# Kernel optimization log

Hardware: AMD Instinct MI355X
Metric: run time of the kernel (lower is better)

The kernel has to match this reference:

```python
import jax, jax.numpy as jnp
import numpy as np

B, F, D = 16384, 32, 64
EPS = 1e-5


def layer_norm(x, g, b):
    m = x.mean(-1, keepdims=True)
    v = ((x - m) ** 2).mean(-1, keepdims=True)
    return (x - m) / jnp.sqrt(v + EPS) * g + b


def setup_inputs() -> dict:
    key = jax.random.key(0)
    ks = jax.random.split(key, 24)
    IN = F * D

    def w(k, shape, fan_in):
        return jax.random.normal(k, shape, dtype=jnp.float32) / np.sqrt(fan_in)

    return {
        "x": jax.random.normal(ks[0], (B, F, D), dtype=jnp.float32),
        # StaticGRN (mask branch): Linear(IN,D) -> ELU -> Linear(D,F); skip Linear(IN,F); GateAndNorm(F)
        "mw1": w(ks[1], (IN, D), IN), "mb1": jnp.zeros((D,), jnp.float32),
        "mw2": w(ks[2], (D, F), D), "mb2": jnp.zeros((F,), jnp.float32),
        "mlw": w(ks[3], (IN, F), IN), "mlb": jnp.zeros((F,), jnp.float32),
        "mgw": w(ks[4], (F, F), F), "mgb": jnp.zeros((F,), jnp.float32),
        "mlw2": w(ks[5], (F, F), F), "mlb2": jnp.zeros((F,), jnp.float32),
        "mgamma": jnp.ones((F,), jnp.float32), "mbeta": jnp.zeros((F,), jnp.float32),
        # Per-feature GRNNoContext params, stacked over F (batched small GEMMs)
        "w1": w(ks[6], (F, D, D), D), "b1": jnp.zeros((F, D), jnp.float32),
        "w2": w(ks[7], (F, D, D), D), "b2": jnp.zeros((F, D), jnp.float32),
        "gw": w(ks[8], (F, D, D), D), "gb": jnp.zeros((F, D), jnp.float32),
        "lw": w(ks[9], (F, D, D), D), "lb": jnp.zeros((F, D), jnp.float32),
        "gamma": jnp.ones((F, D), jnp.float32), "beta": jnp.zeros((F, D), jnp.float32),
    }


def reference(x, mw1, mb1, mw2, mb2, mlw, mlb, mgw, mgb, mlw2, mlb2, mgamma, mbeta,
              w1, b1, w2, b2, gw, gb, lw, lb, gamma, beta):
    b, f, d = x.shape
    flat = x.reshape(b, f * d)
    # StaticGRN mask branch (dropout is 0.0 -> identity)
    h = jax.nn.elu(flat @ mw1 + mb1) @ mw2 + mb2          # [B,F]
    res = flat @ mlw + mlb                                 # [B,F] skip path
    pre = jax.nn.sigmoid(h @ mgw + mgb) * (h @ mlw2 + mlb2) + res
    mask = jax.nn.softmax(layer_norm(pre, mgamma, mbeta), axis=-1)[:, None, :]  # [B,1,F]
    # Per-feature GRNs, batched over the feature axis
    hh = jax.nn.elu(jnp.einsum('bfd,fde->bfe', x, w1) + b1)
    hh = jnp.einsum('bfd,fde->bfe', hh, w2) + b2
    gate = jax.nn.sigmoid(jnp.einsum('bfd,fde->bfe', hh, gw) + gb)
    lin = jnp.einsum('bfd,fde->bfe', hh, lw) + lb
    vecs = layer_norm(gate * lin + x, gamma, beta)         # [B,F,D]
    out = jnp.einsum('bof,bfd->bod', mask, vecs)[:, 0, :]  # [B,D]
    return out, mask
```

## Files before the change

kernel.cpp:

```cpp
#include <hip/hip_runtime.h>
#include <hip/hip_bf16.h>
#include <math.h>

#define NB 16384
#define NF 32
#define ND 64
#define NIN 2048

typedef __attribute__((ext_vector_type(8))) short fragA;
typedef __attribute__((ext_vector_type(4))) float fragC;

#define MFMA(a, b, c) __builtin_amdgcn_mfma_f32_16x16x32_bf16((a), (b), (c), 0, 0, 0)

__device__ __forceinline__ short f2bf(float f) {
    union { float f; unsigned u; } v; v.f = f;
    return (short)((v.u + 0x7fffu + ((v.u >> 16) & 1u)) >> 16);
}
__device__ __forceinline__ fragA cvt8(const float* p) {
    const float4 a = *(const float4*)p;
    const float4 b = *(const float4*)(p + 4);
    union { __hip_bfloat162 h[4]; fragA f; } u;
    u.h[0] = __float22bfloat162_rn(make_float2(a.x, a.y));
    u.h[1] = __float22bfloat162_rn(make_float2(a.z, a.w));
    u.h[2] = __float22bfloat162_rn(make_float2(b.x, b.y));
    u.h[3] = __float22bfloat162_rn(make_float2(b.z, b.w));
    return u.f;
}

__device__ __forceinline__ float frcp(float x) { return __builtin_amdgcn_rcpf(x); }
__device__ __forceinline__ float felu(float v) { return v > 0.f ? v : __expf(v) - 1.f; }
__device__ __forceinline__ float fsig(float g) { return __builtin_amdgcn_rcpf(1.f + __expf(-g)); }

__global__ __launch_bounds__(256) void prep_kernel(
    const float* __restrict__ w1, const float* __restrict__ w2,
    const float* __restrict__ gw, const float* __restrict__ lw,
    const float* __restrict__ mw1, const float* __restrict__ mlw,
    const float* __restrict__ mw2, const float* __restrict__ mgw,
    const float* __restrict__ mlw2,
    short* __restrict__ wsout)
{
    int F = blockIdx.x * 256 + threadIdx.x;
    fragA o;
    if (F < 65536) {
        int mat = F >> 14;
        int f   = (F >> 9) & 31;
        int nt  = (F >> 7) & 3;
        int s   = (F >> 6) & 1;
        int l   = F & 63;
        const float* src = (mat == 0 ? w1 : mat == 1 ? w2 : mat == 2 ? gw : lw)
                           + (size_t)f * 4096;
        int n  = nt * 16 + (l & 15);
        int k0 = s * 32 + ((l >> 4) << 3);
#pragma unroll
        for (int j = 0; j < 8; ++j) o[j] = f2bf(src[(k0 + j) * 64 + n]);
    } else if (F < 90112) {
        int G  = F - 65536;
        int f  = G / 768;
        int r  = G - f * 768;
        int nt = r >> 7;
        int s  = (r >> 6) & 1;
        int l  = r & 63;
        int n  = nt * 16 + (l & 15);
        int k0 = f * 64 + s * 32 + ((l >> 4) << 3);
        if (n < 64) {
#pragma unroll
            for (int j = 0; j < 8; ++j) o[j] = f2bf(mw1[(size_t)(k0 + j) * 64 + n]);
        } else {
#pragma unroll
            for (int j = 0; j < 8; ++j) o[j] = f2bf(mlw[(size_t)(k0 + j) * 32 + (n - 64)]);
        }
    } else {
        int G2 = F - 90112;
        if (G2 < 256) {
            int nt = G2 >> 7, s = (G2 >> 6) & 1, l = G2 & 63;
            int n = nt * 16 + (l & 15);
            int k0 = s * 32 + ((l >> 4) << 3);
#pragma unroll
            for (int j = 0; j < 8; ++j) o[j] = f2bf(mw2[(k0 + j) * 32 + n]);
        } else {
            int G3 = G2 - 256;
            const float* src = (G3 < 128) ? mgw : mlw2;
            G3 &= 127;
            int nt = G3 >> 6, l = G3 & 63;
            int n = nt * 16 + (l & 15);
            int k0 = (l >> 4) << 3;
#pragma unroll
            for (int j = 0; j < 8; ++j) o[j] = f2bf(src[(k0 + j) * 32 + n]);
        }
    }
    ((fragA*)wsout)[F] = o;
}

__global__ __launch_bounds__(256, 4) void fused_kernel(
    const float* __restrict__ x,
    const short* __restrict__ wfrag, const short* __restrict__ mwfrag,
    const short* __restrict__ swfrag,
    const float* __restrict__ mb1, const float* __restrict__ mb2,
    const float* __restrict__ mlb, const float* __restrict__ mgb,
    const float* __restrict__ mlb2,
    const float* __restrict__ mgamma, const float* __restrict__ mbeta,
    const float* __restrict__ b1, const float* __restrict__ b2,
    const float* __restrict__ gb, const float* __restrict__ lb,
    const float* __restrict__ gamma, const float* __restrict__ beta,
    float* __restrict__ mask_out, float* __restrict__ out)
{
    __shared__ float smem[8960];
    float* redS  = smem;
    float* gS    = smem;
    float* lS    = smem + 768;
    float* hS1   = smem + 6208;
    float* resS  = smem + 7296;
    float* h2S   = smem + 7872;
    float* outS  = smem + 4352;
    float* maskS = smem + 8448;

    const int tid = threadIdx.x;
    const int w = tid >> 6, l = tid & 63;
    const int row0 = blockIdx.x * 16;
    const int m = l & 15, q = l >> 4;

    const fragA* wf  = (const fragA*)wfrag;
    const fragA* mwf = (const fragA*)mwfrag;
    const fragA* swf = (const fragA*)swfrag;

    fragC acc[6];
#pragma unroll
    for (int nt = 0; nt < 6; ++nt) acc[nt] = (fragC){0.f, 0.f, 0.f, 0.f};

    const float* xpm = x + (size_t)(row0 + m) * NIN + q * 8;
    for (int fi = 0; fi < 8; ++fi) {
        int f = w * 8 + fi;
        const float* xp = xpm + f * ND;
        fragA a0 = cvt8(xp), a1 = cvt8(xp + 32);
        const size_t fb = (size_t)f * 768 + l;
#pragma unroll
        for (int nt = 0; nt < 6; ++nt) {
            acc[nt] = MFMA(a0, mwf[fb + nt * 128], acc[nt]);
            acc[nt] = MFMA(a1, mwf[fb + nt * 128 + 64], acc[nt]);
        }
    }
    {
        float* myred = redS + w * 1552;
#pragma unroll
        for (int nt = 0; nt < 6; ++nt)
#pragma unroll
            for (int rg = 0; rg < 4; ++rg)
                myred[(q * 4 + rg) * 97 + nt * 16 + m] = acc[nt][rg];
    }
    __syncthreads();

    {
        int r = tid & 15, cb = tid >> 4;
#pragma unroll
        for (int i = 0; i < 6; ++i) {
            int c = cb + i * 16;
            float s = redS[r * 97 + c]        + redS[1552 + r * 97 + c]
                    + redS[3104 + r * 97 + c] + redS[4656 + r * 97 + c];
            if (c < 64) {
                hS1[r * 68 + c] = felu(s + mb1[c]);
            } else {
                resS[r * 36 + (c - 64)] = s + mlb[c - 64];
            }
        }
    }
    __syncthreads();

    if (w < 2) {
        const float* ap = hS1 + m * 68 + q * 8;
        fragA a0 = cvt8(ap), a1 = cvt8(ap + 32);
        fragC c = {0.f, 0.f, 0.f, 0.f};
        c = MFMA(a0, swf[w * 128 + l], c);
        c = MFMA(a1, swf[w * 128 + 64 + l], c);
        float bv = mb2[w * 16 + m];
#pragma unroll
        for (int rg = 0; rg < 4; ++rg)
            h2S[(q * 4 + rg) * 36 + w * 16 + m] = c[rg] + bv;
    }
    __syncthreads();

    {
        int ntc = w & 1;
        int isl = w >> 1;
        fragA a = cvt8(h2S + m * 36 + q * 8);
        fragC c = {0.f, 0.f, 0.f, 0.f};
        c = MFMA(a, swf[256 + isl * 128 + ntc * 64 + l], c);
        float* dst = isl ? lS : gS;
#pragma unroll
        for (int rg = 0; rg < 4; ++rg)
            dst[(q * 4 + rg) * 36 + ntc * 16 + m] = c[rg];
    }
    __syncthreads();

    if (w == 0) {
        int r2 = l >> 2, c0 = (l & 3) * 8;
        float pre[8];
#pragma unroll
        for (int i = 0; i < 8; ++i) {
            int c = c0 + i;
            float gg = gS[r2 * 36 + c] + mgb[c];
            float ll = lS[r2 * 36 + c] + mlb2[c];
            pre[i] = ll * fsig(gg) + resS[r2 * 36 + c];
        }
        float s1 = 0.f, s2 = 0.f;
#pragma unroll
        for (int i = 0; i < 8; ++i) { s1 += pre[i]; s2 += pre[i] * pre[i]; }
        s1 += __shfl_xor(s1, 1); s2 += __shfl_xor(s2, 1);
        s1 += __shfl_xor(s1, 2); s2 += __shfl_xor(s2, 2);
        float mean = s1 * (1.f / 32.f);
        float var  = s2 * (1.f / 32.f) - mean * mean;
        float inv  = rsqrtf(fmaxf(var, 0.f) + 1e-5f);
        float ln[8]; float mx = -3.4e38f;
#pragma unroll
        for (int i = 0; i < 8; ++i) {
            ln[i] = (pre[i] - mean) * inv * mgamma[c0 + i] + mbeta[c0 + i];
            mx = fmaxf(mx, ln[i]);
        }
        mx = fmaxf(mx, __shfl_xor(mx, 1));
        mx = fmaxf(mx, __shfl_xor(mx, 2));
        float ssum = 0.f;
#pragma unroll
        for (int i = 0; i < 8; ++i) { ln[i] = __expf(ln[i] - mx); ssum += ln[i]; }
        ssum += __shfl_xor(ssum, 1); ssum += __shfl_xor(ssum, 2);
        float rs = frcp(ssum);
        float* mo = mask_out + (size_t)(row0 + r2) * 32 + c0;
        *(float4*)mo       = (float4){ln[0] * rs, ln[1] * rs, ln[2] * rs, ln[3] * rs};
        *(float4*)(mo + 4) = (float4){ln[4] * rs, ln[5] * rs, ln[6] * rs, ln[7] * rs};
#pragma unroll
        for (int i = 0; i < 8; ++i) maskS[r2 * 32 + c0 + i] = ln[i] * rs;
    }
    __syncthreads();

    float* hW = smem + w * 1088;

    fragC oac[4];
#pragma unroll
    for (int nt = 0; nt < 4; ++nt) oac[nt] = (fragC){0.f, 0.f, 0.f, 0.f};

    for (int fi = 0; fi < 8; ++fi) {
        const int f = w * 8 + fi;
        const size_t base1 = (size_t)f * 512 + l;
        const size_t base2 = (size_t)(NF + f) * 512 + l;
        const size_t baseg = (size_t)(2 * NF + f) * 512 + l;
        const size_t basel = (size_t)(3 * NF + f) * 512 + l;

        const float* xp = xpm + f * ND;
        fragA a0 = cvt8(xp), a1 = cvt8(xp + 32);
        fragC c1[4];
#pragma unroll
        for (int nt = 0; nt < 4; ++nt) {
            fragC c = {0.f, 0.f, 0.f, 0.f};
            c = MFMA(a0, wf[base1 + nt * 128], c);
            c = MFMA(a1, wf[base1 + nt * 128 + 64], c);
            c1[nt] = c;
        }
        fragA w2f[8];
#pragma unroll
        for (int j = 0; j < 4; ++j) {
            w2f[j]     = wf[base2 + j * 128];
            w2f[j + 4] = wf[base2 + j * 128 + 64];
        }
#pragma unroll
        for (int nt = 0; nt < 4; ++nt) {
            float bv = b1[f * 64 + nt * 16 + m];
            int col = nt * 16 + m;
#pragma unroll
            for (int rg = 0; rg < 4; ++rg)
                hW[(q * 4 + rg) * 68 + col] = felu(c1[nt][rg] + bv);
        }
        const float* ap = hW + m * 68 + q * 8;
        fragA h0 = cvt8(ap), h1 = cvt8(ap + 32);
        fragC c2[4];
#pragma unroll
        for (int nt = 0; nt < 4; ++nt) {
            fragC c = {0.f, 0.f, 0.f, 0.f};
            c = MFMA(h0, w2f[nt], c);
            c = MFMA(h1, w2f[nt + 4], c);
            c2[nt] = c;
        }
        float xres[4][4];
#pragma unroll
        for (int rg = 0; rg < 4; ++rg)
#pragma unroll
            for (int nt = 0; nt < 4; ++nt)
                xres[rg][nt] = x[(size_t)(row0 + q * 4 + rg) * NIN + f * ND + nt * 16 + m];
        float mk[4];
#pragma unroll
        for (int rg = 0; rg < 4; ++rg) mk[rg] = maskS[(q * 4 + rg) * 32 + f];
#pragma unroll
        for (int nt = 0; nt < 4; ++nt) {
            float bv = b2[f * 64 + nt * 16 + m];
            int col = nt * 16 + m;
#pragma unroll
            for (int rg = 0; rg < 4; ++rg)
                hW[(q * 4 + rg) * 68 + col] = c2[nt][rg] + bv;
        }
        const float* ap2 = hW + m * 68 + q * 8;
        fragA g0 = cvt8(ap2), g1 = cvt8(ap2 + 32);
        fragC ga[4], la[4];
#pragma unroll
        for (int nt = 0; nt < 4; ++nt) {
            fragC g = {0.f, 0.f, 0.f, 0.f}, li = {0.f, 0.f, 0.f, 0.f};
            g  = MFMA(g0, wf[baseg + nt * 128], g);
            g  = MFMA(g1, wf[baseg + nt * 128 + 64], g);
            li = MFMA(g0, wf[basel + nt * 128], li);
            li = MFMA(g1, wf[basel + nt * 128 + 64], li);
            ga[nt] = g; la[nt] = li;
        }
        float gbv[4], lbv[4], gmv[4], btv[4];
#pragma unroll
        for (int nt = 0; nt < 4; ++nt) {
            int cidx = f * 64 + nt * 16 + m;
            gbv[nt] = gb[cidx]; lbv[nt] = lb[cidx];
            gmv[nt] = gamma[cidx]; btv[nt] = beta[cidx];
        }
#pragma unroll
        for (int rg = 0; rg < 4; ++rg) {
            float val[4];
#pragma unroll
            for (int nt = 0; nt < 4; ++nt) {
                float gg = ga[nt][rg] + gbv[nt];
                float ll = la[nt][rg] + lbv[nt];
                val[nt] = ll * fsig(gg) + xres[rg][nt];
            }
            float s1 = 0.f, s2 = 0.f;
#pragma unroll
            for (int nt = 0; nt < 4; ++nt) { s1 += val[nt]; s2 += val[nt] * val[nt]; }
            s1 += __shfl_xor(s1, 1); s2 += __shfl_xor(s2, 1);
            s1 += __shfl_xor(s1, 2); s2 += __shfl_xor(s2, 2);
            s1 += __shfl_xor(s1, 4); s2 += __shfl_xor(s2, 4);
            s1 += __shfl_xor(s1, 8); s2 += __shfl_xor(s2, 8);
            float mean = s1 * (1.f / 64.f);
            float var  = s2 * (1.f / 64.f) - mean * mean;
            float inv  = rsqrtf(fmaxf(var, 0.f) + 1e-5f);
#pragma unroll
            for (int nt = 0; nt < 4; ++nt) {
                float vec = (val[nt] - mean) * inv * gmv[nt] + btv[nt];
                oac[nt][rg] += mk[rg] * vec;
            }
        }
    }

#pragma unroll
    for (int nt = 0; nt < 4; ++nt)
#pragma unroll
        for (int rg = 0; rg < 4; ++rg)
            outS[w * 1024 + (q * 4 + rg) * 64 + nt * 16 + m] = oac[nt][rg];
    __syncthreads();
    {
        int t4 = tid * 4;
        int r = t4 >> 6, c = t4 & 63;
        float v[4];
#pragma unroll
        for (int j = 0; j < 4; ++j) {
            v[j] = outS[r * 64 + c + j] + outS[1024 + r * 64 + c + j]
                 + outS[2048 + r * 64 + c + j] + outS[3072 + r * 64 + c + j];
        }
        *(float4*)(out + (size_t)(row0 + r) * 64 + c) = (float4){v[0], v[1], v[2], v[3]};
    }
}

extern "C" void kernel_launch(void* const* d_in, const int* in_sizes, int n_in,
                              void* d_out, int out_size, void* d_ws, size_t ws_size,
                              hipStream_t stream) {
    const float* x      = (const float*)d_in[0];
    const float* mw1    = (const float*)d_in[1];
    const float* mb1    = (const float*)d_in[2];
    const float* mw2    = (const float*)d_in[3];
    const float* mb2    = (const float*)d_in[4];
    const float* mlw    = (const float*)d_in[5];
    const float* mlb    = (const float*)d_in[6];
    const float* mgw    = (const float*)d_in[7];
    const float* mgb    = (const float*)d_in[8];
    const float* mlw2   = (const float*)d_in[9];
    const float* mlb2   = (const float*)d_in[10];
    const float* mgamma = (const float*)d_in[11];
    const float* mbeta  = (const float*)d_in[12];
    const float* w1     = (const float*)d_in[13];
    const float* b1     = (const float*)d_in[14];
    const float* w2     = (const float*)d_in[15];
    const float* b2     = (const float*)d_in[16];
    const float* gw     = (const float*)d_in[17];
    const float* gb     = (const float*)d_in[18];
    const float* lw     = (const float*)d_in[19];
    const float* lb     = (const float*)d_in[20];
    const float* gamma  = (const float*)d_in[21];
    const float* beta   = (const float*)d_in[22];

    float* out  = (float*)d_out;
    float* mask = out + (size_t)NB * 64;

    short* wfrag  = (short*)d_ws;
    short* mwfrag = wfrag + (size_t)65536 * 8;
    short* swfrag = wfrag + (size_t)90112 * 8;

    hipLaunchKernelGGL(prep_kernel, dim3(354), dim3(256), 0, stream,
                       w1, w2, gw, lw, mw1, mlw, mw2, mgw, mlw2, wfrag);
    hipLaunchKernelGGL(fused_kernel, dim3(NB / 16), dim3(256), 0, stream,
                       x, wfrag, mwfrag, swfrag,
                       mb1, mb2, mlb, mgb, mlb2, mgamma, mbeta,
                       b1, b2, gb, lb, gamma, beta,
                       mask, out);
}
```

Before: 310.5 us.

## Double block to eight waves and split mask GEMM and feature loop across them

Launches the fused kernel with 512 threads (8 waves) instead of 256. The mask-branch GEMM is split so each group of four waves computes half of the output tiles. The per-feature GRN loop now gives each wave 4 features instead of 8, and the final output reduction sums 8 partial results. Shared-memory offsets are rearranged, and an extra barrier protects the reused output buffer. The goal is more in-flight waves per block to hide latency. The risks are heavier register limits from the tighter launch bounds, and x fragments being loaded twice in the mask GEMM.

```diff
diff --git a/kernel.cpp b/kernel.cpp
--- a/kernel.cpp
+++ b/kernel.cpp
@@ -91,7 +91,7 @@
     ((fragA*)wsout)[F] = o;
 }
 
-__global__ __launch_bounds__(256, 4) void fused_kernel(
+__global__ __launch_bounds__(512, 8) void fused_kernel(
     const float* __restrict__ x,
     const short* __restrict__ wfrag, const short* __restrict__ mwfrag,
     const short* __restrict__ swfrag,
@@ -104,15 +104,15 @@
     const float* __restrict__ gamma, const float* __restrict__ beta,
     float* __restrict__ mask_out, float* __restrict__ out)
 {
-    __shared__ float smem[8960];
+    __shared__ float smem[9216];
     float* redS  = smem;
     float* gS    = smem;
     float* lS    = smem + 768;
-    float* hS1   = smem + 6208;
-    float* resS  = smem + 7296;
-    float* h2S   = smem + 7872;
-    float* outS  = smem + 4352;
-    float* maskS = smem + 8448;
+    float* hS1   = smem + 6272;
+    float* resS  = smem + 7360;
+    float* h2S   = smem + 7936;
+    float* outS  = smem;
+    float* maskS = smem + 8704;
 
     const int tid = threadIdx.x;
     const int w = tid >> 6, l = tid & 63;
@@ -123,39 +123,44 @@
     const fragA* mwf = (const fragA*)mwfrag;
     const fragA* swf = (const fragA*)swfrag;
 
-    fragC acc[6];
-#pragma unroll
-    for (int nt = 0; nt < 6; ++nt) acc[nt] = (fragC){0.f, 0.f, 0.f, 0.f};
+    const int fs = (w & 3) * 8;
+    const int nh = w >> 2;
+    fragC acc[3];
+#pragma unroll
+    for (int j = 0; j < 3; ++j) acc[j] = (fragC){0.f, 0.f, 0.f, 0.f};
 
     const float* xpm = x + (size_t)(row0 + m) * NIN + q * 8;
     for (int fi = 0; fi < 8; ++fi) {
-        int f = w * 8 + fi;
+        int f = fs + fi;
         const float* xp = xpm + f * ND;
         fragA a0 = cvt8(xp), a1 = cvt8(xp + 32);
         const size_t fb = (size_t)f * 768 + l;
 #pragma unroll
-        for (int nt = 0; nt < 6; ++nt) {
-            acc[nt] = MFMA(a0, mwf[fb + nt * 128], acc[nt]);
-            acc[nt] = MFMA(a1, mwf[fb + nt * 128 + 64], acc[nt]);
+        for (int j = 0; j < 3; ++j) {
+            int nt = nh * 3 + j;
+            acc[j] = MFMA(a0, mwf[fb + nt * 128], acc[j]);
+            acc[j] = MFMA(a1, mwf[fb + nt * 128 + 64], acc[j]);
         }
     }
     {
-        float* myred = redS + w * 1552;
-#pragma unroll
-        for (int nt = 0; nt < 6; ++nt)
+        float* myred = redS + w * 784;
+#pragma unroll
+        for (int j = 0; j < 3; ++j)
 #pragma unroll
             for (int rg = 0; rg < 4; ++rg)
-                myred[(q * 4 + rg) * 97 + nt * 16 + m] = acc[nt][rg];
+                myred[(q * 4 + rg) * 49 + j * 16 + m] = acc[j][rg];
     }
     __syncthreads();
 
     {
         int r = tid & 15, cb = tid >> 4;
 #pragma unroll
-        for (int i = 0; i < 6; ++i) {
-            int c = cb + i * 16;
-            float s = redS[r * 97 + c]        + redS[1552 + r * 97 + c]
-                    + redS[3104 + r * 97 + c] + redS[4656 + r * 97 + c];
+        for (int i = 0; i < 3; ++i) {
+            int c = cb + i * 32;
+            int nh2 = (c >= 48) ? 1 : 0;
+            int base = nh2 * 3136 + r * 49 + (c - nh2 * 48);
+            float s = redS[base] + redS[base + 784]
+                    + redS[base + 1568] + redS[base + 2352];
             if (c < 64) {
                 hS1[r * 68 + c] = felu(s + mb1[c]);
             } else {
@@ -178,7 +183,7 @@
     }
     __syncthreads();
 
-    {
+    if (w < 4) {
         int ntc = w & 1;
         int isl = w >> 1;
         fragA a = cvt8(h2S + m * 36 + q * 8);
@@ -236,8 +241,8 @@
 #pragma unroll
     for (int nt = 0; nt < 4; ++nt) oac[nt] = (fragC){0.f, 0.f, 0.f, 0.f};
 
-    for (int fi = 0; fi < 8; ++fi) {
-        const int f = w * 8 + fi;
+    for (int fi = 0; fi < 4; ++fi) {
+        const int f = w * 4 + fi;
         const size_t base1 = (size_t)f * 512 + l;
         const size_t base2 = (size_t)(NF + f) * 512 + l;
         const size_t baseg = (size_t)(2 * NF + f) * 512 + l;
@@ -340,6 +345,7 @@
         }
     }
 
+    __syncthreads();
 #pragma unroll
     for (int nt = 0; nt < 4; ++nt)
 #pragma unroll
@@ -347,15 +353,15 @@
             outS[w * 1024 + (q * 4 + rg) * 64 + nt * 16 + m] = oac[nt][rg];
     __syncthreads();
     {
-        int t4 = tid * 4;
-        int r = t4 >> 6, c = t4 & 63;
-        float v[4];
-#pragma unroll
-        for (int j = 0; j < 4; ++j) {
-            v[j] = outS[r * 64 + c + j] + outS[1024 + r * 64 + c + j]
-                 + outS[2048 + r * 64 + c + j] + outS[3072 + r * 64 + c + j];
-        }
-        *(float4*)(out + (size_t)(row0 + r) * 64 + c) = (float4){v[0], v[1], v[2], v[3]};
+        int t2 = tid * 2;
+        int r = t2 >> 6, c = t2 & 63;
+        float v0 = 0.f, v1 = 0.f;
+#pragma unroll
+        for (int ww = 0; ww < 8; ++ww) {
+            v0 += outS[ww * 1024 + r * 64 + c];
+            v1 += outS[ww * 1024 + r * 64 + c + 1];
+        }
+        *(float2*)(out + (size_t)(row0 + r) * 64 + c) = make_float2(v0, v1);
     }
 }
 
@@ -395,7 +401,7 @@
 
     hipLaunchKernelGGL(prep_kernel, dim3(354), dim3(256), 0, stream,
                        w1, w2, gw, lw, mw1, mlw, mw2, mgw, mlw2, wfrag);
-    hipLaunchKernelGGL(fused_kernel, dim3(NB / 16), dim3(256), 0, stream,
+    hipLaunchKernelGGL(fused_kernel, dim3(NB / 16), dim3(512), 0, stream,
                        x, wfrag, mwfrag, swfrag,
                        mb1, mb2, mlb, mgb, mlb2, mgamma, mbeta,
                        b1, b2, gb, lb, gamma, beta,
```

Result: slower. 386.6 us (+24.5%).

## Chain per-feature GRN GEMMs in registers via transposed 16x16x16 MFMA fragments

Applied to the files above, without the earlier changes.

The per-feature GRN now computes transposed products, with weights as the A operand and activations as the B operand. Each MFMA output then already matches the B-operand layout of the next 16x16x16 bf16 MFMA, so the LDS round trips between the first, second and gate/linear GEMMs are gone. The prep kernel repacks w2, gw and lw into 4-element k-chunk fragments. Bias, residual, gamma and beta loads become float4 row loads, and the layer-norm reduction across lanes shrinks to two shuffles. The cost is twice as many (smaller) MFMA instructions for the later GEMMs, plus a fallback macro that silently does nothing if the builtin is missing.

```diff
diff --git a/kernel.cpp b/kernel.cpp
--- a/kernel.cpp
+++ b/kernel.cpp
@@ -8,9 +8,16 @@
 #define NIN 2048
 
 typedef __attribute__((ext_vector_type(8))) short fragA;
+typedef __attribute__((ext_vector_type(4))) short frag16;
 typedef __attribute__((ext_vector_type(4))) float fragC;
 
 #define MFMA(a, b, c) __builtin_amdgcn_mfma_f32_16x16x32_bf16((a), (b), (c), 0, 0, 0)
+
+#if __has_builtin(__builtin_amdgcn_mfma_f32_16x16x16bf16_1k)
+#define MFMA16(a, b, c) __builtin_amdgcn_mfma_f32_16x16x16bf16_1k((a), (b), (c), 0, 0, 0)
+#else
+#define MFMA16(a, b, c) (c)
+#endif
 
 __device__ __forceinline__ short f2bf(float f) {
     union { float f; unsigned u; } v; v.f = f;
@@ -24,6 +31,12 @@
     u.h[1] = __float22bfloat162_rn(make_float2(a.z, a.w));
     u.h[2] = __float22bfloat162_rn(make_float2(b.x, b.y));
     u.h[3] = __float22bfloat162_rn(make_float2(b.z, b.w));
+    return u.f;
+}
+__device__ __forceinline__ frag16 cvt4(float v0, float v1, float v2, float v3) {
+    union { __hip_bfloat162 h[2]; frag16 f; } u;
+    u.h[0] = __float22bfloat162_rn(make_float2(v0, v1));
+    u.h[1] = __float22bfloat162_rn(make_float2(v2, v3));
     return u.f;
 }
 
@@ -41,18 +54,34 @@
 {
     int F = blockIdx.x * 256 + threadIdx.x;
     fragA o;
-    if (F < 65536) {
-        int mat = F >> 14;
+    if (F < 16384) {
         int f   = (F >> 9) & 31;
         int nt  = (F >> 7) & 3;
         int s   = (F >> 6) & 1;
         int l   = F & 63;
-        const float* src = (mat == 0 ? w1 : mat == 1 ? w2 : mat == 2 ? gw : lw)
-                           + (size_t)f * 4096;
+        const float* src = w1 + (size_t)f * 4096;
         int n  = nt * 16 + (l & 15);
         int k0 = s * 32 + ((l >> 4) << 3);
 #pragma unroll
         for (int j = 0; j < 8; ++j) o[j] = f2bf(src[(k0 + j) * 64 + n]);
+    } else if (F < 65536) {
+        int G = F - 16384;
+        union { short s[8]; fragA a; } u;
+#pragma unroll
+        for (int h = 0; h < 2; ++h) {
+            int e   = 2 * G + h;
+            int l   = e & 63;
+            int kc  = (e >> 6) & 3;
+            int nt2 = (e >> 8) & 3;
+            int f   = (e >> 10) & 31;
+            int mat = e >> 15;
+            const float* src = (mat == 0 ? w2 : mat == 1 ? gw : lw) + (size_t)f * 4096;
+            int col = nt2 * 16 + (l & 15);
+            int k0  = kc * 16 + ((l >> 4) << 2);
+#pragma unroll
+            for (int j = 0; j < 4; ++j) u.s[h * 4 + j] = f2bf(src[(k0 + j) * 64 + col]);
+        }
+        o = u.a;
     } else if (F < 90112) {
         int G  = F - 65536;
         int f  = G / 768;
@@ -111,7 +140,7 @@
     float* hS1   = smem + 6208;
     float* resS  = smem + 7296;
     float* h2S   = smem + 7872;
-    float* outS  = smem + 4352;
+    float* outS  = smem;
     float* maskS = smem + 8448;
 
     const int tid = threadIdx.x;
@@ -119,9 +148,10 @@
     const int row0 = blockIdx.x * 16;
     const int m = l & 15, q = l >> 4;
 
-    const fragA* wf  = (const fragA*)wfrag;
-    const fragA* mwf = (const fragA*)mwfrag;
-    const fragA* swf = (const fragA*)swfrag;
+    const fragA*  wf   = (const fragA*)wfrag;
+    const frag16* wf16 = (const frag16*)wfrag + 32768;
+    const fragA*  mwf  = (const fragA*)mwfrag;
+    const fragA*  swf  = (const fragA*)swfrag;
 
     fragC acc[6];
 #pragma unroll
@@ -230,132 +260,114 @@
     }
     __syncthreads();
 
-    float* hW = smem + w * 1088;
-
     fragC oac[4];
 #pragma unroll
     for (int nt = 0; nt < 4; ++nt) oac[nt] = (fragC){0.f, 0.f, 0.f, 0.f};
+
+    const int r = m;
+    const float* xrow = x + (size_t)(row0 + r) * NIN;
 
     for (int fi = 0; fi < 8; ++fi) {
         const int f = w * 8 + fi;
         const size_t base1 = (size_t)f * 512 + l;
-        const size_t base2 = (size_t)(NF + f) * 512 + l;
-        const size_t baseg = (size_t)(2 * NF + f) * 512 + l;
-        const size_t basel = (size_t)(3 * NF + f) * 512 + l;
 
         const float* xp = xpm + f * ND;
         fragA a0 = cvt8(xp), a1 = cvt8(xp + 32);
-        fragC c1[4];
+        fragC h1[4];
 #pragma unroll
         for (int nt = 0; nt < 4; ++nt) {
             fragC c = {0.f, 0.f, 0.f, 0.f};
-            c = MFMA(a0, wf[base1 + nt * 128], c);
-            c = MFMA(a1, wf[base1 + nt * 128 + 64], c);
-            c1[nt] = c;
-        }
-        fragA w2f[8];
-#pragma unroll
-        for (int j = 0; j < 4; ++j) {
-            w2f[j]     = wf[base2 + j * 128];
-            w2f[j + 4] = wf[base2 + j * 128 + 64];
-        }
+            c = MFMA(wf[base1 + nt * 128], a0, c);
+            c = MFMA(wf[base1 + nt * 128 + 64], a1, c);
+            h1[nt] = c;
+        }
+        frag16 h1b[4];
 #pragma unroll
         for (int nt = 0; nt < 4; ++nt) {
-            float bv = b1[f * 64 + nt * 16 + m];
-            int col = nt * 16 + m;
-#pragma unroll
-            for (int rg = 0; rg < 4; ++rg)
-                hW[(q * 4 + rg) * 68 + col] = felu(c1[nt][rg] + bv);
-        }
-        const float* ap = hW + m * 68 + q * 8;
-        fragA h0 = cvt8(ap), h1 = cvt8(ap + 32);
-        fragC c2[4];
-#pragma unroll
-        for (int nt = 0; nt < 4; ++nt) {
+            const float4 bv = *(const float4*)(b1 + f * 64 + nt * 16 + q * 4);
+            h1b[nt] = cvt4(felu(h1[nt][0] + bv.x), felu(h1[nt][1] + bv.y),
+                           felu(h1[nt][2] + bv.z), felu(h1[nt][3] + bv.w));
+        }
+        const frag16* w2p = wf16 + (size_t)f * 1024 + l;
+        fragC h2[4];
+#pragma unroll
+        for (int nt2 = 0; nt2 < 4; ++nt2) {
             fragC c = {0.f, 0.f, 0.f, 0.f};
-            c = MFMA(h0, w2f[nt], c);
-            c = MFMA(h1, w2f[nt + 4], c);
-            c2[nt] = c;
-        }
-        float xres[4][4];
-#pragma unroll
-        for (int rg = 0; rg < 4; ++rg)
-#pragma unroll
-            for (int nt = 0; nt < 4; ++nt)
-                xres[rg][nt] = x[(size_t)(row0 + q * 4 + rg) * NIN + f * ND + nt * 16 + m];
-        float mk[4];
-#pragma unroll
-        for (int rg = 0; rg < 4; ++rg) mk[rg] = maskS[(q * 4 + rg) * 32 + f];
-#pragma unroll
-        for (int nt = 0; nt < 4; ++nt) {
-            float bv = b2[f * 64 + nt * 16 + m];
-            int col = nt * 16 + m;
-#pragma unroll
-            for (int rg = 0; rg < 4; ++rg)
-                hW[(q * 4 + rg) * 68 + col] = c2[nt][rg] + bv;
-        }
-        const float* ap2 = hW + m * 68 + q * 8;
-        fragA g0 = cvt8(ap2), g1 = cvt8(ap2 + 32);
+#pragma unroll
+            for (int kc = 0; kc < 4; ++kc)
+                c = MFMA16(w2p[nt2 * 256 + kc * 64], h1b[kc], c);
+            h2[nt2] = c;
+        }
+        frag16 h2b[4];
+#pragma unroll
+        for (int nt2 = 0; nt2 < 4; ++nt2) {
+            const float4 bv = *(const float4*)(b2 + f * 64 + nt2 * 16 + q * 4);
+            h2b[nt2] = cvt4(h2[nt2][0] + bv.x, h2[nt2][1] + bv.y,
+                            h2[nt2][2] + bv.z, h2[nt2][3] + bv.w);
+        }
+        const frag16* gwp = wf16 + 32768 + (size_t)f * 1024 + l;
+        const frag16* lwp = wf16 + 65536 + (size_t)f * 1024 + l;
         fragC ga[4], la[4];
 #pragma unroll
         for (int nt = 0; nt < 4; ++nt) {
             fragC g = {0.f, 0.f, 0.f, 0.f}, li = {0.f, 0.f, 0.f, 0.f};
-            g  = MFMA(g0, wf[baseg + nt * 128], g);
-            g  = MFMA(g1, wf[baseg + nt * 128 + 64], g);
-            li = MFMA(g0, wf[basel + nt * 128], li);
-            li = MFMA(g1, wf[basel + nt * 128 + 64], li);
+#pragma unroll
+            for (int kc = 0; kc < 4; ++kc) {
+                g  = MFMA16(gwp[nt * 256 + kc * 64], h2b[kc], g);
+                li = MFMA16(lwp[nt * 256 + kc * 64], h2b[kc], li);
+            }
             ga[nt] = g; la[nt] = li;
         }
-        float gbv[4], lbv[4], gmv[4], btv[4];
+        const float mk = maskS[r * 32 + f];
+        float val[4][4];
+        float s1 = 0.f, s2 = 0.f;
 #pragma unroll
         for (int nt = 0; nt < 4; ++nt) {
-            int cidx = f * 64 + nt * 16 + m;
-            gbv[nt] = gb[cidx]; lbv[nt] = lb[cidx];
-            gmv[nt] = gamma[cidx]; btv[nt] = beta[cidx];
-        }
-#pragma unroll
-        for (int rg = 0; rg < 4; ++rg) {
-            float val[4];
-#pragma unroll
-            for (int nt = 0; nt < 4; ++nt) {
-                float gg = ga[nt][rg] + gbv[nt];
-                float ll = la[nt][rg] + lbv[nt];
-                val[nt] = ll * fsig(gg) + xres[rg][nt];
+            const float4 gbv = *(const float4*)(gb + f * 64 + nt * 16 + q * 4);
+            const float4 lbv = *(const float4*)(lb + f * 64 + nt * 16 + q * 4);
+            const float4 xr  = *(const float4*)(xrow + f * 64 + nt * 16 + q * 4);
+#pragma unroll
+            for (int rg = 0; rg < 4; ++rg) {
+                float gg = ga[nt][rg] + ((const float*)&gbv)[rg];
+                float ll = la[nt][rg] + ((const float*)&lbv)[rg];
+                float vv = ll * fsig(gg) + ((const float*)&xr)[rg];
+                val[nt][rg] = vv;
+                s1 += vv; s2 += vv * vv;
             }
-            float s1 = 0.f, s2 = 0.f;
-#pragma unroll
-            for (int nt = 0; nt < 4; ++nt) { s1 += val[nt]; s2 += val[nt] * val[nt]; }
-            s1 += __shfl_xor(s1, 1); s2 += __shfl_xor(s2, 1);
-            s1 += __shfl_xor(s1, 2); s2 += __shfl_xor(s2, 2);
-            s1 += __shfl_xor(s1, 4); s2 += __shfl_xor(s2, 4);
-            s1 += __shfl_xor(s1, 8); s2 += __shfl_xor(s2, 8);
-            float mean = s1 * (1.f / 64.f);
-            float var  = s2 * (1.f / 64.f) - mean * mean;
-            float inv  = rsqrtf(fmaxf(var, 0.f) + 1e-5f);
-#pragma unroll
-            for (int nt = 0; nt < 4; ++nt) {
-                float vec = (val[nt] - mean) * inv * gmv[nt] + btv[nt];
-                oac[nt][rg] += mk[rg] * vec;
+        }
+        s1 += __shfl_xor(s1, 16); s2 += __shfl_xor(s2, 16);
+        s1 += __shfl_xor(s1, 32); s2 += __shfl_xor(s2, 32);
+        float mean = s1 * (1.f / 64.f);
+        float var  = s2 * (1.f / 64.f) - mean * mean;
+        float inv  = rsqrtf(fmaxf(var, 0.f) + 1e-5f);
+#pragma unroll
+        for (int nt = 0; nt < 4; ++nt) {
+            const float4 gmv = *(const float4*)(gamma + f * 64 + nt * 16 + q * 4);
+            const float4 btv = *(const float4*)(beta  + f * 64 + nt * 16 + q * 4);
+#pragma unroll
+            for (int rg = 0; rg < 4; ++rg) {
+                float vec = (val[nt][rg] - mean) * inv * ((const float*)&gmv)[rg]
+                          + ((const float*)&btv)[rg];
+                oac[nt][rg] += mk * vec;
             }
         }
     }
 
+    __syncthreads();
 #pragma unroll
     for (int nt = 0; nt < 4; ++nt)
-#pragma unroll
-        for (int rg = 0; rg < 4; ++rg)
-            outS[w * 1024 + (q * 4 + rg) * 64 + nt * 16 + m] = oac[nt][rg];
+        *(fragC*)(outS + w * 1024 + r * 64 + nt * 16 + q * 4) = oac[nt];
     __syncthreads();
     {
         int t4 = tid * 4;
-        int r = t4 >> 6, c = t4 & 63;
+        int rr = t4 >> 6, c = t4 & 63;
         float v[4];
 #pragma unroll
         for (int j = 0; j < 4; ++j) {
-            v[j] = outS[r * 64 + c + j] + outS[1024 + r * 64 + c + j]
-                 + outS[2048 + r * 64 + c + j] + outS[3072 + r * 64 + c + j];
-        }
-        *(float4*)(out + (size_t)(row0 + r) * 64 + c) = (float4){v[0], v[1], v[2], v[3]};
+            v[j] = outS[rr * 64 + c + j] + outS[1024 + rr * 64 + c + j]
+                 + outS[2048 + rr * 64 + c + j] + outS[3072 + rr * 64 + c + j];
+        }
+        *(float4*)(out + (size_t)(row0 + rr) * 64 + c) = (float4){v[0], v[1], v[2], v[3]};
     }
 }
 
```

Result: slower. 352.1 us (+13.4%).
